# Kernel optimization log

Hardware: AMD Instinct MI355X
Metric: run time of the kernel (lower is better)

The kernel has to match this reference:

```python
import jax, jax.numpy as jnp
import numpy as np

NUM_GROUPS = 8
NUM_HEADS = 8
EPS = 1e-5


def setup_inputs() -> dict:
    key = jax.random.key(0)
    k1, k2, k3 = jax.random.split(key, 3)
    b, c, h, w = 16, 512, 32, 32
    x = jax.random.normal(k1, (b, c, h, w), dtype=jnp.float32)
    gn_w = jnp.ones((c,), dtype=jnp.float32)
    gn_b = jnp.zeros((c,), dtype=jnp.float32)
    qkv_w = jax.random.normal(k2, (3 * c, c), dtype=jnp.float32) * (1.0 / np.sqrt(c))
    qkv_b = jnp.zeros((3 * c,), dtype=jnp.float32)
    proj_w = jax.random.normal(k3, (c, c), dtype=jnp.float32) * (1.0 / np.sqrt(c))
    proj_b = jnp.zeros((c,), dtype=jnp.float32)
    return {"x": x, "gn_w": gn_w, "gn_b": gn_b, "qkv_w": qkv_w,
            "qkv_b": qkv_b, "proj_w": proj_w, "proj_b": proj_b}


def reference(x, gn_w, gn_b, qkv_w, qkv_b, proj_w, proj_b):
    b, c, h, w = x.shape
    H = NUM_HEADS
    d = c // H
    N = h * w
    scale = d ** (-0.5)

    # GroupNorm(8, c), affine
    xg = x.reshape(b, NUM_GROUPS, -1)
    mu = xg.mean(axis=-1, keepdims=True)
    var = xg.var(axis=-1, keepdims=True)
    xn = ((xg - mu) * jax.lax.rsqrt(var + EPS)).reshape(b, c, h, w)
    xn = xn * gn_w[None, :, None, None] + gn_b[None, :, None, None]

    # 1x1 conv qkv: [b, 3c, h, w]
    qkv = jnp.einsum('oc,bchw->bohw', qkv_w, xn) + qkv_b[None, :, None, None]
    # 'b (three h d) x y -> three b h (x y) d'
    qkv = qkv.reshape(b, 3, H, d, N)          # (b, 3, H, d, N)
    q = jnp.swapaxes(qkv[:, 0], -1, -2)       # (b, H, N, d)
    k = jnp.swapaxes(qkv[:, 1], -1, -2)
    v = jnp.swapaxes(qkv[:, 2], -1, -2)

    attn = jnp.einsum('bhid,bhjd->bhij', q, k) * scale
    attn = jax.nn.softmax(attn, axis=-1)
    out = jnp.einsum('bhij,bhjd->bhid', attn, v)  # (b, H, N, d)

    # 'b h (x y) d -> b (h d) x y'
    out = jnp.swapaxes(out, -1, -2).reshape(b, c, h, w)
    out = jnp.einsum('oc,bchw->bohw', proj_w, out) + proj_b[None, :, None, None]
    return x + out
```

## Files before the change

kernel.cpp:

```cpp
#include <hip/hip_runtime.h>
#include <math.h>

typedef unsigned short u16;
typedef __attribute__((ext_vector_type(8))) short short8;
typedef __attribute__((ext_vector_type(4))) float floatx4;
typedef __attribute__((ext_vector_type(4))) u16 v4u16;
typedef __attribute__((ext_vector_type(8))) u16 v8u16;

#define B_   16
#define C_   512
#define NSP  1024
#define EPSV 1e-5f
#define QSCALE 0.18033688011117f

__device__ __forceinline__ u16 f2bf(float f) {
  union { float f; unsigned u; } v; v.f = f;
  unsigned r = v.u + 0x7FFFu + ((v.u >> 16) & 1u);
  return (u16)(r >> 16);
}

__device__ __forceinline__ void gld16(const u16* g, u16* l) {
  __builtin_amdgcn_global_load_lds(
      (const __attribute__((address_space(1))) void*)g,
      (__attribute__((address_space(3))) void*)l, 16, 0, 0);
}

__device__ __forceinline__ short8 lds_read_b128(const u16* p) {
  short8 r;
  asm volatile("ds_read_b128 %0, %1"
               : "=&v"(r)
               : "v"((const __attribute__((address_space(3))) u16*)p));
  return r;
}

__device__ __forceinline__ unsigned pk_bf(float a, float b) {
  return __builtin_amdgcn_perm(__float_as_uint(b), __float_as_uint(a), 0x07060302u);
}

__global__ __launch_bounds__(256) void cvt_bf16(
    const float* __restrict__ qa, u16* __restrict__ oa,
    const float* __restrict__ pa, u16* __restrict__ ob)
{
  int blk = blockIdx.x;
  const float* in; u16* out; int i;
  if (blk < 768) { in = qa; out = oa; i = (blk * 256 + threadIdx.x) * 4; }
  else           { in = pa; out = ob; i = ((blk - 768) * 256 + threadIdx.x) * 4; }
  float4 v = *(const float4*)(in + i);
  v4u16 o = { f2bf(v.x), f2bf(v.y), f2bf(v.z), f2bf(v.w) };
  *(v4u16*)(out + i) = o;
}

__global__ __launch_bounds__(256) void gn_stats(
    const float* __restrict__ x, float* __restrict__ stats)
{
  int blk = blockIdx.x;
  int bg = blk >> 3, ck = blk & 7;
  const float4* xp = (const float4*)(x + (((size_t)bg * 64 + ck * 8) * NSP));
  float s = 0.f, ss = 0.f;
#pragma unroll
  for (int it = 0; it < 8; ++it) {
    float4 v = xp[it * 256 + threadIdx.x];
    s  += v.x + v.y + v.z + v.w;
    ss += v.x * v.x + v.y * v.y + v.z * v.z + v.w * v.w;
  }
  for (int off = 32; off > 0; off >>= 1) {
    s  += __shfl_down(s, off);
    ss += __shfl_down(ss, off);
  }
  __shared__ float rs[4], rss[4];
  int lane = threadIdx.x & 63, wv = threadIdx.x >> 6;
  if (lane == 0) { rs[wv] = s; rss[wv] = ss; }
  __syncthreads();
  if (threadIdx.x == 0) {
    float S  = rs[0] + rs[1] + rs[2] + rs[3];
    float SS = rss[0] + rss[1] + rss[2] + rss[3];
    atomicAdd(&stats[bg * 2], S);
    atomicAdd(&stats[bg * 2 + 1], SS);
  }
}

__global__ __launch_bounds__(256) void gn_apply(
    const float* __restrict__ x, const float* __restrict__ stats,
    const float* __restrict__ gw, const float* __restrict__ gb,
    u16* __restrict__ xn)
{
  int blk = blockIdx.x;
  int bg = blk >> 4, nt = blk & 15;
  int b = bg >> 3, g = bg & 7;
  float S = stats[bg * 2], SS = stats[bg * 2 + 1];
  float mu  = S * (1.f / 65536.f);
  float var = SS * (1.f / 65536.f) - mu * mu;
  float inv = rsqrtf(var + EPSV);
  __shared__ float T[64][65];
  const float* xb = x + (size_t)bg * 64 * NSP;
  int t = threadIdx.x;
#pragma unroll
  for (int it = 0; it < 4; ++it) {
    int task = it * 256 + t;
    int cc = task >> 4, ns = task & 15;
    float4 v = *(const float4*)(xb + (size_t)cc * NSP + nt * 64 + ns * 4);
    T[cc][ns * 4 + 0] = v.x; T[cc][ns * 4 + 1] = v.y;
    T[cc][ns * 4 + 2] = v.z; T[cc][ns * 4 + 3] = v.w;
  }
  __syncthreads();
#pragma unroll
  for (int it = 0; it < 2; ++it) {
    int task = it * 256 + t;
    int n = task >> 3, cs = task & 7;
    v8u16 o;
#pragma unroll
    for (int u = 0; u < 8; ++u) {
      int cg = g * 64 + cs * 8 + u;
      float val = (T[cs * 8 + u][n] - mu) * inv * gw[cg] + gb[cg];
      o[u] = f2bf(val);
    }
    *(v8u16*)(xn + ((size_t)b * NSP + nt * 64 + n) * C_ + g * 64 + cs * 8) = o;
  }
}

template <int MODE>
__global__ __launch_bounds__(256) void gemm_mfma(
    const u16* __restrict__ W, const u16* __restrict__ X,
    const float* __restrict__ bias, const float* __restrict__ resid,
    u16* __restrict__ out_qk, u16* __restrict__ out_v,
    float* __restrict__ out_f)
{
  __shared__ u16 smem[24576];
  int id = blockIdx.x;
  int yb = id >> 7, rr = id & 127;
  int b = rr >> 3, xb_ = rr & 7;
  int m0 = yb * 128, n0 = xb_ * 128;
  int t = threadIdx.x, lane = t & 63, w = t >> 6;
  int c = lane & 15, q = lane >> 4;
  int wm = w >> 1, wn = w & 1;
  const u16* Xb = X + (size_t)b * NSP * C_;

  floatx4 acc[4][4];
#pragma unroll
  for (int mi = 0; mi < 4; ++mi)
#pragma unroll
    for (int ni = 0; ni < 4; ++ni) acc[mi][ni] = (floatx4){0.f, 0.f, 0.f, 0.f};

  auto stage = [&](int buf, int k0) {
    u16* Asb = smem + buf * 8192;
    u16* Bsb = Asb + 4096;
#pragma unroll
    for (int it = 0; it < 2; ++it) {
      int task = it * 256 + t;
      int mr = task >> 2;
      int gk = (task & 3) ^ ((mr >> 1) & 3);
      gld16(W + (size_t)(m0 + mr) * C_ + k0 + gk * 8, Asb + task * 8);
    }
#pragma unroll
    for (int it = 0; it < 2; ++it) {
      int task = it * 256 + t;
      int nr = task >> 2;
      int gk = (task & 3) ^ ((nr >> 1) & 3);
      gld16(Xb + (size_t)(n0 + nr) * C_ + k0 + gk * 8, Bsb + task * 8);
    }
  };

  auto compute = [&](int buf) {
    const u16* As = smem + buf * 8192;
    const u16* Bs = As + 4096;
    short8 af[4], bfr[4];
#pragma unroll
    for (int mi = 0; mi < 4; ++mi) {
      int m = wm * 64 + mi * 16 + c;
      af[mi] = lds_read_b128(As + m * 32 + ((q ^ ((m >> 1) & 3)) << 3));
    }
#pragma unroll
    for (int ni = 0; ni < 4; ++ni) {
      int n = wn * 64 + ni * 16 + c;
      bfr[ni] = lds_read_b128(Bs + n * 32 + ((q ^ ((n >> 1) & 3)) << 3));
    }
    asm volatile("s_waitcnt lgkmcnt(0)" ::: "memory");
    __builtin_amdgcn_sched_barrier(0);
#pragma unroll
    for (int mi = 0; mi < 4; ++mi)
#pragma unroll
      for (int ni = 0; ni < 4; ++ni)
        acc[mi][ni] = __builtin_amdgcn_mfma_f32_16x16x32_bf16(
            af[mi], bfr[ni], acc[mi][ni], 0, 0, 0);
  };

  stage(0, 0);
  stage(1, 32);
  int cur = 0, tgt = 2;
  for (int ki = 0; ki < 14; ++ki) {
    asm volatile("s_waitcnt vmcnt(4)" ::: "memory");
    __builtin_amdgcn_s_barrier();
    stage(tgt, (ki + 2) * 32);
    compute(cur);
    cur = (cur == 2) ? 0 : cur + 1;
    tgt = (tgt == 2) ? 0 : tgt + 1;
  }
  asm volatile("s_waitcnt vmcnt(4)" ::: "memory");
  __builtin_amdgcn_s_barrier();
  compute(2);
  asm volatile("s_waitcnt vmcnt(0)" ::: "memory");
  __builtin_amdgcn_s_barrier();
  compute(0);
  __syncthreads();

  if (MODE == 0) {
    if (m0 < 1024) {
      float sc = (m0 < 512) ? QSCALE : 1.0f;
      u16* Cl = smem;
#pragma unroll
      for (int mi = 0; mi < 4; ++mi) {
        floatx4 bi = *(const floatx4*)(bias + m0 + wm * 64 + mi * 16 + q * 4);
#pragma unroll
        for (int ni = 0; ni < 4; ++ni) {
          int n = wn * 64 + ni * 16 + c;
          int m = wm * 64 + mi * 16 + q * 4;
          v4u16 pk;
#pragma unroll
          for (int r = 0; r < 4; ++r) pk[r] = f2bf((acc[mi][ni][r] + bi[r]) * sc);
          *(v4u16*)(Cl + n * 136 + m) = pk;
        }
      }
      __syncthreads();
#pragma unroll
      for (int it = 0; it < 8; ++it) {
        int task = it * 256 + t;
        int n = task >> 4, seg = task & 15;
        v8u16 v = *(const v8u16*)(Cl + n * 136 + seg * 8);
        *(v8u16*)(out_qk + ((size_t)b * NSP + n0 + n) * 1024 + m0 + seg * 8) = v;
      }
    } else {
      u16* Cl = smem;
#pragma unroll
      for (int mi = 0; mi < 4; ++mi) {
        floatx4 bi = *(const floatx4*)(bias + m0 + wm * 64 + mi * 16 + q * 4);
#pragma unroll
        for (int ni = 0; ni < 4; ++ni) {
          int n = wn * 64 + ni * 16 + c;
          int m = wm * 64 + mi * 16 + q * 4;
#pragma unroll
          for (int r = 0; r < 4; ++r)
            Cl[(m + r) * 136 + n] = f2bf(acc[mi][ni][r] + bi[r]);
        }
      }
      __syncthreads();
#pragma unroll
      for (int it = 0; it < 8; ++it) {
        int task = it * 256 + t;
        int m = task >> 4, seg = task & 15;
        int g64 = seg >> 3, s = seg & 7;
        int k0 = ((s & 4) << 3) | ((s & 1) << 4) | ((s & 2) << 1);
        v8u16 v = *(const v8u16*)(Cl + m * 136 + seg * 8);
        v4u16 lo = { v[0], v[1], v[2], v[3] };
        v4u16 hi = { v[4], v[5], v[6], v[7] };
        size_t base = ((size_t)b * C_ + m0 - 1024 + m) * NSP + n0 + g64 * 64;
        *(v4u16*)(out_v + base + k0) = lo;
        *(v4u16*)(out_v + base + k0 + 8) = hi;
      }
    }
  } else {
#pragma unroll
    for (int mi = 0; mi < 4; ++mi) {
      floatx4 bi = *(const floatx4*)(bias + m0 + wm * 64 + mi * 16 + q * 4);
#pragma unroll
      for (int ni = 0; ni < 4; ++ni) {
        int n = n0 + wn * 64 + ni * 16 + c;
        int m = m0 + wm * 64 + mi * 16 + q * 4;
#pragma unroll
        for (int r = 0; r < 4; ++r) {
          size_t o = ((size_t)b * C_ + m + r) * NSP + n;
          out_f[o] = acc[mi][ni][r] + bi[r] + resid[o];
        }
      }
    }
  }
}

__global__ __launch_bounds__(256, 4) void attn_mfma(
    const u16* __restrict__ qk, const u16* __restrict__ vbuf,
    u16* __restrict__ att)
{
  __shared__ u16 __align__(16) smem[16384];
  int id = blockIdx.x;
  int hb = id & 127;
  int i0 = id >> 7;
  int h = hb >> 4, b = hb & 15;
  int t = threadIdx.x, lane = t & 63, w = t >> 6;
  int c = lane & 15, q = lane >> 4;
  const u16* qbase = qk + (size_t)b * NSP * 1024;
  const u16* vbase = vbuf + (size_t)(b * C_ + h * 64) * NSP;

#pragma unroll
  for (int it = 0; it < 4; ++it) {
    int task = it * 256 + t;
    int r = task >> 3, seg = task & 7, ds = (seg ^ (r & 7)) * 8;
    gld16(qbase + (size_t)(i0 * 128 + r) * 1024 + h * 64 + ds, smem + task * 8);
  }
#pragma unroll
  for (int it = 0; it < 2; ++it) {
    int task = it * 256 + t;
    int r = task >> 3, seg = task & 7, ds = (seg ^ (r & 7)) * 8;
    gld16(qbase + (size_t)r * 1024 + 512 + h * 64 + ds, smem + 8192 + task * 8);
    gld16(vbase + (size_t)r * NSP + ds, smem + 12288 + task * 8);
  }
  __syncthreads();

  short8 qa[2][2];
#pragma unroll
  for (int nf = 0; nf < 2; ++nf) {
    int row = w * 32 + nf * 16 + c;
#pragma unroll
    for (int ch = 0; ch < 2; ++ch)
      qa[nf][ch] = *(const short8*)(smem + row * 64 + (((q + 4 * ch) ^ (c & 7)) << 3));
  }
  __syncthreads();

  short8 onesf;
#pragma unroll
  for (int u = 0; u < 8; ++u) onesf[u] = (short)0x3F80;

  floatx4 Oacc[4][2];
  floatx4 OaccT[2];
#pragma unroll
  for (int dt = 0; dt < 4; ++dt)
#pragma unroll
    for (int nf = 0; nf < 2; ++nf) Oacc[dt][nf] = (floatx4){0.f, 0.f, 0.f, 0.f};
#pragma unroll
  for (int nf = 0; nf < 2; ++nf) OaccT[nf] = (floatx4){0.f, 0.f, 0.f, 0.f};

  for (int j0 = 0; j0 < 16; ++j0) {
    int p = j0 & 1;
    u16* KS = smem + (p ? 0 : 8192);
    u16* VS = KS + 4096;
    if (j0 < 15) {
      u16* KN = smem + (p ? 8192 : 0);
      u16* VN = KN + 4096;
#pragma unroll
      for (int it = 0; it < 2; ++it) {
        int task = it * 256 + t;
        int r = task >> 3, seg = task & 7, ds = (seg ^ (r & 7)) * 8;
        gld16(qbase + (size_t)((j0 + 1) * 64 + r) * 1024 + 512 + h * 64 + ds,
              KN + task * 8);
        gld16(vbase + (size_t)r * NSP + (j0 + 1) * 64 + ds, VN + task * 8);
      }
    }
#pragma unroll
    for (int jt2 = 0; jt2 < 2; ++jt2) {
      short8 kb[2][2], vf[4];
#pragma unroll
      for (int jj = 0; jj < 2; ++jj) {
        int row = (jt2 * 2 + jj) * 16 + c;
        kb[jj][0] = lds_read_b128(KS + row * 64 + ((q ^ (row & 7)) << 3));
        kb[jj][1] = lds_read_b128(KS + row * 64 + (((q + 4) ^ (row & 7)) << 3));
      }
#pragma unroll
      for (int dt = 0; dt < 4; ++dt) {
        int dd = dt * 16 + c;
        vf[dt] = lds_read_b128(VS + dd * 64 + (((jt2 * 4 + q) ^ (dd & 7)) << 3));
      }
      asm volatile("s_waitcnt lgkmcnt(0)" ::: "memory");
      __builtin_amdgcn_sched_barrier(0);
      unsigned pk2[2][2][2];
#pragma unroll
      for (int jj = 0; jj < 2; ++jj) {
#pragma unroll
        for (int nf = 0; nf < 2; ++nf) {
          floatx4 z = (floatx4){0.f, 0.f, 0.f, 0.f};
          z = __builtin_amdgcn_mfma_f32_16x16x32_bf16(kb[jj][0], qa[nf][0], z, 0, 0, 0);
          z = __builtin_amdgcn_mfma_f32_16x16x32_bf16(kb[jj][1], qa[nf][1], z, 0, 0, 0);
          float p0 = __builtin_amdgcn_exp2f(z[0]);
          float p1 = __builtin_amdgcn_exp2f(z[1]);
          float p2 = __builtin_amdgcn_exp2f(z[2]);
          float p3 = __builtin_amdgcn_exp2f(z[3]);
          pk2[jj][nf][0] = pk_bf(p0, p1);
          pk2[jj][nf][1] = pk_bf(p2, p3);
        }
      }
      short8 pf[2];
#pragma unroll
      for (int nf = 0; nf < 2; ++nf) {
        union { short8 s; unsigned d[4]; } u;
        u.d[0] = pk2[0][nf][0]; u.d[1] = pk2[0][nf][1];
        u.d[2] = pk2[1][nf][0]; u.d[3] = pk2[1][nf][1];
        pf[nf] = u.s;
      }
      __builtin_amdgcn_s_setprio(1);
#pragma unroll
      for (int dt = 0; dt < 4; ++dt)
#pragma unroll
        for (int nf = 0; nf < 2; ++nf)
          Oacc[dt][nf] = __builtin_amdgcn_mfma_f32_16x16x32_bf16(
              vf[dt], pf[nf], Oacc[dt][nf], 0, 0, 0);
#pragma unroll
      for (int nf = 0; nf < 2; ++nf)
        OaccT[nf] = __builtin_amdgcn_mfma_f32_16x16x32_bf16(
            onesf, pf[nf], OaccT[nf], 0, 0, 0);
      __builtin_amdgcn_s_setprio(0);
    }
    __syncthreads();
  }

#pragma unroll
  for (int nf = 0; nf < 2; ++nf) {
    float rinv = 1.f / OaccT[nf][0];
    int n = i0 * 128 + w * 32 + nf * 16 + c;
#pragma unroll
    for (int dt = 0; dt < 4; ++dt) {
      v4u16 pk;
#pragma unroll
      for (int r = 0; r < 4; ++r) pk[r] = f2bf(Oacc[dt][nf][r] * rinv);
      *(v4u16*)(att + ((size_t)b * NSP + n) * C_ + h * 64 + dt * 16 + q * 4) = pk;
    }
  }
}

extern "C" void kernel_launch(void* const* d_in, const int* in_sizes, int n_in,
                              void* d_out, int out_size, void* d_ws, size_t ws_size,
                              hipStream_t stream)
{
  const float* x    = (const float*)d_in[0];
  const float* gw   = (const float*)d_in[1];
  const float* gb   = (const float*)d_in[2];
  const float* qkvw = (const float*)d_in[3];
  const float* qkvb = (const float*)d_in[4];
  const float* pw   = (const float*)d_in[5];
  const float* pb   = (const float*)d_in[6];
  float* out = (float*)d_out;

  u16* xn    = (u16*)d_ws;
  u16* qkb   = xn   + 8388608;
  u16* vbf   = qkb  + 16777216;
  u16* attb  = vbf  + 8388608;
  u16* wq    = attb + 8388608;
  u16* wp    = wq   + 786432;
  float* stats = (float*)(wp + 262144);

  hipMemsetAsync(stats, 0, 128 * 2 * sizeof(float), stream);
  cvt_bf16<<<1024, 256, 0, stream>>>(qkvw, wq, pw, wp);
  gn_stats<<<1024, 256, 0, stream>>>(x, stats);
  gn_apply<<<2048, 256, 0, stream>>>(x, stats, gw, gb, xn);
  gemm_mfma<0><<<dim3(1536), 256, 0, stream>>>(
      wq, xn, qkvb, nullptr, qkb, vbf, nullptr);
  attn_mfma<<<dim3(1024), 256, 0, stream>>>(qkb, vbf, attb);
  gemm_mfma<1><<<dim3(512), 256, 0, stream>>>(
      wp, attb, pb, x, nullptr, nullptr, out);
}
```

Baseline: 195.4 us.

## Split attention query tile across eight waves with 16 rows each

The attention kernel moves from 256 to 512 threads per block, so each of the eight waves owns 16 query rows instead of 32. K/V tile loads are now spread over twice as many threads, with one 16-byte load each per tile. This gives more waves to hide latency and lowers per-wave register pressure. In exchange each wave rereads the same K/V fragments from LDS for half as many queries, which doubles LDS read traffic per useful MFMA, and launch bounds of 512x4 may cap registers.

```diff
diff --git a/kernel.cpp b/kernel.cpp
--- a/kernel.cpp
+++ b/kernel.cpp
@@ -275,7 +275,7 @@
   }
 }
 
-__global__ __launch_bounds__(256, 4) void attn_mfma(
+__global__ __launch_bounds__(512, 4) void attn_mfma(
     const u16* __restrict__ qk, const u16* __restrict__ vbuf,
     u16* __restrict__ att)
 {
@@ -290,27 +290,24 @@
   const u16* vbase = vbuf + (size_t)(b * C_ + h * 64) * NSP;
 
 #pragma unroll
-  for (int it = 0; it < 4; ++it) {
-    int task = it * 256 + t;
+  for (int it = 0; it < 2; ++it) {
+    int task = it * 512 + t;
     int r = task >> 3, seg = task & 7, ds = (seg ^ (r & 7)) * 8;
     gld16(qbase + (size_t)(i0 * 128 + r) * 1024 + h * 64 + ds, smem + task * 8);
   }
-#pragma unroll
-  for (int it = 0; it < 2; ++it) {
-    int task = it * 256 + t;
-    int r = task >> 3, seg = task & 7, ds = (seg ^ (r & 7)) * 8;
-    gld16(qbase + (size_t)r * 1024 + 512 + h * 64 + ds, smem + 8192 + task * 8);
-    gld16(vbase + (size_t)r * NSP + ds, smem + 12288 + task * 8);
+  {
+    int r = t >> 3, seg = t & 7, ds = (seg ^ (r & 7)) * 8;
+    gld16(qbase + (size_t)r * 1024 + 512 + h * 64 + ds, smem + 8192 + t * 8);
+    gld16(vbase + (size_t)r * NSP + ds, smem + 12288 + t * 8);
   }
   __syncthreads();
 
-  short8 qa[2][2];
-#pragma unroll
-  for (int nf = 0; nf < 2; ++nf) {
-    int row = w * 32 + nf * 16 + c;
+  short8 qa[2];
+  {
+    int row = w * 16 + c;
 #pragma unroll
     for (int ch = 0; ch < 2; ++ch)
-      qa[nf][ch] = *(const short8*)(smem + row * 64 + (((q + 4 * ch) ^ (c & 7)) << 3));
+      qa[ch] = *(const short8*)(smem + row * 64 + (((q + 4 * ch) ^ (c & 7)) << 3));
   }
   __syncthreads();
 
@@ -318,14 +315,11 @@
 #pragma unroll
   for (int u = 0; u < 8; ++u) onesf[u] = (short)0x3F80;
 
-  floatx4 Oacc[4][2];
-  floatx4 OaccT[2];
-#pragma unroll
-  for (int dt = 0; dt < 4; ++dt)
-#pragma unroll
-    for (int nf = 0; nf < 2; ++nf) Oacc[dt][nf] = (floatx4){0.f, 0.f, 0.f, 0.f};
-#pragma unroll
-  for (int nf = 0; nf < 2; ++nf) OaccT[nf] = (floatx4){0.f, 0.f, 0.f, 0.f};
+  floatx4 Oacc[4];
+  floatx4 OaccT;
+#pragma unroll
+  for (int dt = 0; dt < 4; ++dt) Oacc[dt] = (floatx4){0.f, 0.f, 0.f, 0.f};
+  OaccT = (floatx4){0.f, 0.f, 0.f, 0.f};
 
   for (int j0 = 0; j0 < 16; ++j0) {
     int p = j0 & 1;
@@ -334,14 +328,10 @@
     if (j0 < 15) {
       u16* KN = smem + (p ? 8192 : 0);
       u16* VN = KN + 4096;
-#pragma unroll
-      for (int it = 0; it < 2; ++it) {
-        int task = it * 256 + t;
-        int r = task >> 3, seg = task & 7, ds = (seg ^ (r & 7)) * 8;
-        gld16(qbase + (size_t)((j0 + 1) * 64 + r) * 1024 + 512 + h * 64 + ds,
-              KN + task * 8);
-        gld16(vbase + (size_t)r * NSP + (j0 + 1) * 64 + ds, VN + task * 8);
-      }
+      int r = t >> 3, seg = t & 7, ds = (seg ^ (r & 7)) * 8;
+      gld16(qbase + (size_t)((j0 + 1) * 64 + r) * 1024 + 512 + h * 64 + ds,
+            KN + t * 8);
+      gld16(vbase + (size_t)r * NSP + (j0 + 1) * 64 + ds, VN + t * 8);
     }
 #pragma unroll
     for (int jt2 = 0; jt2 < 2; ++jt2) {
@@ -359,55 +349,45 @@
       }
       asm volatile("s_waitcnt lgkmcnt(0)" ::: "memory");
       __builtin_amdgcn_sched_barrier(0);
-      unsigned pk2[2][2][2];
+      unsigned pk2[2][2];
 #pragma unroll
       for (int jj = 0; jj < 2; ++jj) {
-#pragma unroll
-        for (int nf = 0; nf < 2; ++nf) {
-          floatx4 z = (floatx4){0.f, 0.f, 0.f, 0.f};
-          z = __builtin_amdgcn_mfma_f32_16x16x32_bf16(kb[jj][0], qa[nf][0], z, 0, 0, 0);
-          z = __builtin_amdgcn_mfma_f32_16x16x32_bf16(kb[jj][1], qa[nf][1], z, 0, 0, 0);
-          float p0 = __builtin_amdgcn_exp2f(z[0]);
-          float p1 = __builtin_amdgcn_exp2f(z[1]);
-          float p2 = __builtin_amdgcn_exp2f(z[2]);
-          float p3 = __builtin_amdgcn_exp2f(z[3]);
-          pk2[jj][nf][0] = pk_bf(p0, p1);
-          pk2[jj][nf][1] = pk_bf(p2, p3);
-        }
-      }
-      short8 pf[2];
-#pragma unroll
-      for (int nf = 0; nf < 2; ++nf) {
+        floatx4 z = (floatx4){0.f, 0.f, 0.f, 0.f};
+        z = __builtin_amdgcn_mfma_f32_16x16x32_bf16(kb[jj][0], qa[0], z, 0, 0, 0);
+        z = __builtin_amdgcn_mfma_f32_16x16x32_bf16(kb[jj][1], qa[1], z, 0, 0, 0);
+        float p0 = __builtin_amdgcn_exp2f(z[0]);
+        float p1 = __builtin_amdgcn_exp2f(z[1]);
+        float p2 = __builtin_amdgcn_exp2f(z[2]);
+        float p3 = __builtin_amdgcn_exp2f(z[3]);
+        pk2[jj][0] = pk_bf(p0, p1);
+        pk2[jj][1] = pk_bf(p2, p3);
+      }
+      short8 pf;
+      {
         union { short8 s; unsigned d[4]; } u;
-        u.d[0] = pk2[0][nf][0]; u.d[1] = pk2[0][nf][1];
-        u.d[2] = pk2[1][nf][0]; u.d[3] = pk2[1][nf][1];
-        pf[nf] = u.s;
+        u.d[0] = pk2[0][0]; u.d[1] = pk2[0][1];
+        u.d[2] = pk2[1][0]; u.d[3] = pk2[1][1];
+        pf = u.s;
       }
       __builtin_amdgcn_s_setprio(1);
 #pragma unroll
       for (int dt = 0; dt < 4; ++dt)
-#pragma unroll
-        for (int nf = 0; nf < 2; ++nf)
-          Oacc[dt][nf] = __builtin_amdgcn_mfma_f32_16x16x32_bf16(
-              vf[dt], pf[nf], Oacc[dt][nf], 0, 0, 0);
-#pragma unroll
-      for (int nf = 0; nf < 2; ++nf)
-        OaccT[nf] = __builtin_amdgcn_mfma_f32_16x16x32_bf16(
-            onesf, pf[nf], OaccT[nf], 0, 0, 0);
+        Oacc[dt] = __builtin_amdgcn_mfma_f32_16x16x32_bf16(
+            vf[dt], pf, Oacc[dt], 0, 0, 0);
+      OaccT = __builtin_amdgcn_mfma_f32_16x16x32_bf16(onesf, pf, OaccT, 0, 0, 0);
       __builtin_amdgcn_s_setprio(0);
     }
     __syncthreads();
   }
 
-#pragma unroll
-  for (int nf = 0; nf < 2; ++nf) {
-    float rinv = 1.f / OaccT[nf][0];
-    int n = i0 * 128 + w * 32 + nf * 16 + c;
+  {
+    float rinv = 1.f / OaccT[0];
+    int n = i0 * 128 + w * 16 + c;
 #pragma unroll
     for (int dt = 0; dt < 4; ++dt) {
       v4u16 pk;
 #pragma unroll
-      for (int r = 0; r < 4; ++r) pk[r] = f2bf(Oacc[dt][nf][r] * rinv);
+      for (int r = 0; r < 4; ++r) pk[r] = f2bf(Oacc[dt][r] * rinv);
       *(v4u16*)(att + ((size_t)b * NSP + n) * C_ + h * 64 + dt * 16 + q * 4) = pk;
     }
   }
@@ -440,7 +420,7 @@
   gn_apply<<<2048, 256, 0, stream>>>(x, stats, gw, gb, xn);
   gemm_mfma<0><<<dim3(1536), 256, 0, stream>>>(
       wq, xn, qkvb, nullptr, qkb, vbf, nullptr);
-  attn_mfma<<<dim3(1024), 256, 0, stream>>>(qkb, vbf, attb);
+  attn_mfma<<<dim3(1024), 512, 0, stream>>>(qkb, vbf, attb);
   gemm_mfma<1><<<dim3(512), 256, 0, stream>>>(
       wp, attb, pb, x, nullptr, nullptr, out);
 }
```

Result: slower. 202.2 us (+3.5%).

## Software-pipeline PV MFMAs one step behind QK/exp in attention loop

Applied to the files above, without the earlier changes.

Restructures the attention inner loop so the P·V and row-sum MFMAs for the previous sub-tile run while the current tile's K/V LDS reads are in flight. The softmax exp and bf16 packing of the current tile are then held in registers until the next step. The V fragments and P values are double-buffered in registers, with a drain after the loop. Launch bounds are relaxed from 4 to 3 blocks per CU so the extra live registers fit. This trades occupancy for better overlap of LDS latency, exp and matrix work.

```diff
diff --git a/kernel.cpp b/kernel.cpp
--- a/kernel.cpp
+++ b/kernel.cpp
@@ -275,7 +275,7 @@
   }
 }
 
-__global__ __launch_bounds__(256, 4) void attn_mfma(
+__global__ __launch_bounds__(256, 3) void attn_mfma(
     const u16* __restrict__ qk, const u16* __restrict__ vbuf,
     u16* __restrict__ att)
 {
@@ -327,6 +327,14 @@
 #pragma unroll
   for (int nf = 0; nf < 2; ++nf) OaccT[nf] = (floatx4){0.f, 0.f, 0.f, 0.f};
 
+  short8 vf2[2][4], pf2[2][2];
+#pragma unroll
+  for (int i = 0; i < 4; ++i)
+    vf2[1][i] = (short8){0, 0, 0, 0, 0, 0, 0, 0};
+#pragma unroll
+  for (int i = 0; i < 2; ++i)
+    pf2[1][i] = (short8){0, 0, 0, 0, 0, 0, 0, 0};
+
   for (int j0 = 0; j0 < 16; ++j0) {
     int p = j0 & 1;
     u16* KS = smem + (p ? 0 : 8192);
@@ -345,7 +353,11 @@
     }
 #pragma unroll
     for (int jt2 = 0; jt2 < 2; ++jt2) {
-      short8 kb[2][2], vf[4];
+      short8 (&vfc)[4] = vf2[jt2];
+      short8 (&vfp)[4] = vf2[jt2 ^ 1];
+      short8 (&pfc)[2] = pf2[jt2];
+      short8 (&pfp)[2] = pf2[jt2 ^ 1];
+      short8 kb[2][2];
 #pragma unroll
       for (int jj = 0; jj < 2; ++jj) {
         int row = (jt2 * 2 + jj) * 16 + c;
@@ -355,8 +367,21 @@
 #pragma unroll
       for (int dt = 0; dt < 4; ++dt) {
         int dd = dt * 16 + c;
-        vf[dt] = lds_read_b128(VS + dd * 64 + (((jt2 * 4 + q) ^ (dd & 7)) << 3));
-      }
+        vfc[dt] = lds_read_b128(VS + dd * 64 + (((jt2 * 4 + q) ^ (dd & 7)) << 3));
+      }
+      __builtin_amdgcn_sched_barrier(0);
+      __builtin_amdgcn_s_setprio(1);
+#pragma unroll
+      for (int dt = 0; dt < 4; ++dt)
+#pragma unroll
+        for (int nf = 0; nf < 2; ++nf)
+          Oacc[dt][nf] = __builtin_amdgcn_mfma_f32_16x16x32_bf16(
+              vfp[dt], pfp[nf], Oacc[dt][nf], 0, 0, 0);
+#pragma unroll
+      for (int nf = 0; nf < 2; ++nf)
+        OaccT[nf] = __builtin_amdgcn_mfma_f32_16x16x32_bf16(
+            onesf, pfp[nf], OaccT[nf], 0, 0, 0);
+      __builtin_amdgcn_s_setprio(0);
       asm volatile("s_waitcnt lgkmcnt(0)" ::: "memory");
       __builtin_amdgcn_sched_barrier(0);
       unsigned pk2[2][2][2];
@@ -375,29 +400,29 @@
           pk2[jj][nf][1] = pk_bf(p2, p3);
         }
       }
-      short8 pf[2];
 #pragma unroll
       for (int nf = 0; nf < 2; ++nf) {
         union { short8 s; unsigned d[4]; } u;
         u.d[0] = pk2[0][nf][0]; u.d[1] = pk2[0][nf][1];
         u.d[2] = pk2[1][nf][0]; u.d[3] = pk2[1][nf][1];
-        pf[nf] = u.s;
-      }
-      __builtin_amdgcn_s_setprio(1);
-#pragma unroll
-      for (int dt = 0; dt < 4; ++dt)
-#pragma unroll
-        for (int nf = 0; nf < 2; ++nf)
-          Oacc[dt][nf] = __builtin_amdgcn_mfma_f32_16x16x32_bf16(
-              vf[dt], pf[nf], Oacc[dt][nf], 0, 0, 0);
-#pragma unroll
-      for (int nf = 0; nf < 2; ++nf)
-        OaccT[nf] = __builtin_amdgcn_mfma_f32_16x16x32_bf16(
-            onesf, pf[nf], OaccT[nf], 0, 0, 0);
-      __builtin_amdgcn_s_setprio(0);
+        pfc[nf] = u.s;
+      }
     }
     __syncthreads();
   }
+
+  __builtin_amdgcn_s_setprio(1);
+#pragma unroll
+  for (int dt = 0; dt < 4; ++dt)
+#pragma unroll
+    for (int nf = 0; nf < 2; ++nf)
+      Oacc[dt][nf] = __builtin_amdgcn_mfma_f32_16x16x32_bf16(
+          vf2[1][dt], pf2[1][nf], Oacc[dt][nf], 0, 0, 0);
+#pragma unroll
+  for (int nf = 0; nf < 2; ++nf)
+    OaccT[nf] = __builtin_amdgcn_mfma_f32_16x16x32_bf16(
+        onesf, pf2[1][nf], OaccT[nf], 0, 0, 0);
+  __builtin_amdgcn_s_setprio(0);
 
 #pragma unroll
   for (int nf = 0; nf < 2; ++nf) {
```

Measured after the change: 198.2 us. About the same (+1.4%).
